# Kernel tuning notes

Measured on AMD Instinct MI355X. Metric: run time of the kernel, lower is better.

## Reference

```python
import jax, jax.numpy as jnp
import numpy as np

B, S, H = 1, 4096, 3584
NQ, NKV, D = 16, 8, 256
N_REP = NQ // NKV  # GQA repeat factor = 2
WINDOW = 2048
SOFTCAP = 50.0
THETA = 10000.0
SCALE = D ** -0.5


def rotate_half(x):
    h = x.shape[-1] // 2
    return jnp.concatenate([-x[..., h:], x[..., :h]], axis=-1)


def setup_inputs() -> dict:
    key = jax.random.key(0)
    k0, k1, k2, k3, k4 = jax.random.split(key, 5)
    return {
        "hidden_states": jax.random.normal(k0, (B, S, H), jnp.float32),
        "wq": jax.random.normal(k1, (H, NQ * D), jnp.float32) / np.sqrt(H).astype(np.float32),
        "wk": jax.random.normal(k2, (H, NKV * D), jnp.float32) / np.sqrt(H).astype(np.float32),
        "wv": jax.random.normal(k3, (H, NKV * D), jnp.float32) / np.sqrt(H).astype(np.float32),
        "wo": jax.random.normal(k4, (NQ * D, H), jnp.float32) / np.sqrt(NQ * D).astype(np.float32),
        "position_ids": jnp.arange(S, dtype=jnp.int64 if jax.config.jax_enable_x64 else jnp.int32)[None, :],
    }


def reference(hidden_states, wq, wk, wv, wo, position_ids):
    b, s, h = hidden_states.shape
    # QKV projections (no bias, per attention_bias=False)
    q = (hidden_states @ wq).reshape(b, s, NQ, D).transpose(0, 2, 1, 3)   # [b, nq, s, d]
    k = (hidden_states @ wk).reshape(b, s, NKV, D).transpose(0, 2, 1, 3)  # [b, nkv, s, d]
    v = (hidden_states @ wv).reshape(b, s, NKV, D).transpose(0, 2, 1, 3)

    # Rotary embeddings (Gemma2RotaryEmbedding): freqs duplicated, rotate_half form
    pos = position_ids.astype(jnp.float32)                         # [b, s]
    inv_freq = 1.0 / (THETA ** (jnp.arange(0, D, 2, dtype=jnp.float32) / D))  # [d/2]
    freqs = pos[..., None] * inv_freq                              # [b, s, d/2]
    emb = jnp.concatenate([freqs, freqs], axis=-1)                 # [b, s, d]
    cos = jnp.cos(emb)[:, None, :, :]                              # [b, 1, s, d]
    sin = jnp.sin(emb)[:, None, :, :]
    q = q * cos + rotate_half(q) * sin
    k = k * cos + rotate_half(k) * sin

    # GQA: repeat_kv (repeat_interleave over head dim)
    k = jnp.repeat(k, N_REP, axis=1)  # [b, nq, s, d]
    v = jnp.repeat(v, N_REP, axis=1)

    # scaled scores + logit softcapping
    scores = jnp.einsum('bhqd,bhkd->bhqk', q, k) * SCALE
    scores = SOFTCAP * jnp.tanh(scores / SOFTCAP)

    # causal + sliding-window mask built from positions
    qpos = position_ids[:, None, :, None]  # [b,1,s,1]
    kpos = position_ids[:, None, None, :]  # [b,1,1,s]
    visible = (kpos <= qpos) & (kpos > qpos - WINDOW)
    scores = jnp.where(visible, scores, jnp.finfo(scores.dtype).min)

    attn = jax.nn.softmax(scores, axis=-1)
    out = jnp.einsum('bhqk,bhkd->bhqd', attn, v)      # [b, nq, s, d]
    out = out.transpose(0, 2, 1, 3).reshape(b, s, NQ * D)
    return out @ wo                                    # [b, s, h]
```

## Files before the change

kernel.cpp:

```cpp
#include <hip/hip_runtime.h>
#include <hip/hip_bf16.h>
#include <cstdint>
#include <cstddef>

#define DEVFN __device__ __forceinline__

typedef __attribute__((ext_vector_type(4))) float f32x4;
typedef __attribute__((ext_vector_type(8))) short bf16x8;
typedef __attribute__((ext_vector_type(4))) short short4v;
typedef __attribute__((ext_vector_type(8))) short short8v;

static constexpr int S = 4096;
static constexpr int H = 3584;
static constexpr int NQ = 16;
static constexpr int NKV = 8;
static constexpr int D = 256;
static constexpr int WINDOW = 2048;
static constexpr float SCALE = 0.0625f;

DEVFN unsigned short f2bf(float f) {
  __hip_bfloat16 h = __float2bfloat16(f);
  return __builtin_bit_cast(unsigned short, h);
}
DEVFN float bf2f(unsigned short h) {
  union { uint32_t u; float f; } x; x.u = ((uint32_t)h) << 16;
  return x.f;
}

DEVFN void load_lds16(const void* g, void* l) {
  __builtin_amdgcn_global_load_lds((const __attribute__((address_space(1))) void*)g,
                                   (__attribute__((address_space(3))) void*)l,
                                   16, 0, 0);
}

__global__ __launch_bounds__(256) void cast_hs_kernel(const float* __restrict__ in,
                                                      unsigned short* __restrict__ out) {
  int i = (blockIdx.x * 256 + threadIdx.x) * 8;
  float4 a = *(const float4*)(in + i);
  float4 b = *(const float4*)(in + i + 4);
  short8v o;
  o[0] = (short)f2bf(a.x); o[1] = (short)f2bf(a.y);
  o[2] = (short)f2bf(a.z); o[3] = (short)f2bf(a.w);
  o[4] = (short)f2bf(b.x); o[5] = (short)f2bf(b.y);
  o[6] = (short)f2bf(b.z); o[7] = (short)f2bf(b.w);
  *(short8v*)(out + i) = o;
}

__global__ __launch_bounds__(256) void transpose_cast_kernel(const float* __restrict__ in,
                                                             unsigned short* __restrict__ out,
                                                             int rows, int cols, int out_ld) {
  __shared__ float tile[64][65];
  const int r0 = blockIdx.y * 64, c0 = blockIdx.x * 64;
  const int t = threadIdx.x;
  const int rr = t >> 4, c4 = (t & 15) * 4;
#pragma unroll
  for (int j = 0; j < 4; ++j) {
    float4 v = *(const float4*)(in + (size_t)(r0 + rr + j * 16) * cols + c0 + c4);
    tile[rr + j * 16][c4 + 0] = v.x;
    tile[rr + j * 16][c4 + 1] = v.y;
    tile[rr + j * 16][c4 + 2] = v.z;
    tile[rr + j * 16][c4 + 3] = v.w;
  }
  __syncthreads();
  const int c = t >> 2, ch = (t & 3) * 16;
  short8v o0, o1;
#pragma unroll
  for (int j = 0; j < 8; ++j) o0[j] = (short)f2bf(tile[ch + j][c]);
#pragma unroll
  for (int j = 0; j < 8; ++j) o1[j] = (short)f2bf(tile[ch + 8 + j][c]);
  unsigned short* dst = out + (size_t)(c0 + c) * out_ld + r0 + ch;
  *(short8v*)dst = o0;
  *(short8v*)(dst + 8) = o1;
}

__global__ __launch_bounds__(256) void rope_table_kernel(float* __restrict__ cs) {
  int idx = blockIdx.x * 256 + threadIdx.x;
  int s = idx >> 7, i = idx & 127;
  float inv = exp2f((float)i * -0.10381025296523007f);
  float f = (float)s * inv;
  cs[idx] = cosf(f);
  cs[(S * 128) + idx] = sinf(f);
}

DEVFN void gemm256_mainloop(const unsigned short* __restrict__ A,
                            const unsigned short* __restrict__ Bt,
                            int Kdim, int lda, int ldb, int row0, int col0,
                            char* lds, f32x4 acc[8][4]) {
  const int tid = threadIdx.x, lane = tid & 63;
  const int w = tid >> 6;
  const int wm = w >> 2, wn = w & 3;
  const int NT = Kdim >> 6;

  const int u = ((tid & 7) * 16) ^ (((tid >> 3) & 7) << 4);
  const int srow = (tid >> 3) + (u >> 6) * 128;
  const int sc = (u & 63) >> 1;

  const unsigned short* aSrc = A + (size_t)(row0 + srow) * lda + sc;
  const unsigned short* bSrc = Bt + (size_t)(col0 + srow) * ldb + sc;
  const size_t aj = (size_t)64 * lda, bj = (size_t)64 * ldb;

  char* const dA = lds + tid * 16;
  char* const dB = lds + 32768 + tid * 16;

  const int aoff = (lane & 15) * 128 + ((((lane >> 4) * 16) + wm * 64) ^ ((lane & 7) << 4));
  const int boff = ((wn & 1) * 64 + (lane & 15)) * 128 +
                   ((((lane >> 4) * 16) + (wn >> 1) * 64) ^ ((lane & 7) << 4));

#define STAGE_A(kt2, kh) do { \
    char* d_ = dA + (((kt2) & 1) << 16) + ((kh) << 14); \
    const unsigned short* s_ = aSrc + (kt2) * 64 + (kh) * 32; \
    load_lds16(s_, d_); load_lds16(s_ + aj, d_ + 8192); } while (0)
#define STAGE_B(kt2, kh) do { \
    char* d_ = dB + (((kt2) & 1) << 16) + ((kh) << 14); \
    const unsigned short* s_ = bSrc + (kt2) * 64 + (kh) * 32; \
    load_lds16(s_, d_); load_lds16(s_ + bj, d_ + 8192); } while (0)

  STAGE_A(0, 0); STAGE_B(0, 0); STAGE_A(0, 1); STAGE_B(0, 1);
  if (NT > 1) { STAGE_A(1, 0); STAGE_B(1, 0); }
  asm volatile("s_waitcnt vmcnt(4)" ::: "memory");
  __builtin_amdgcn_s_barrier();
  asm volatile("" ::: "memory");

  for (int kt = 0; kt < NT; ++kt) {
    const char* lA = lds + ((kt & 1) << 16) + aoff;
    const char* lB = lds + ((kt & 1) << 16) + 32768 + boff;
    bf16x8 bfr[4];
#pragma unroll
    for (int ph = 0; ph < 4; ++ph) {
      const int kh = ph >> 1;
      const int mh = ph & 1;
      bf16x8 af[4];
#pragma unroll
      for (int j = 0; j < 4; ++j)
        af[j] = *(const bf16x8*)(lA + (kh << 14) + (mh * 4 + j) * 2048);
      if (mh == 0) {
#pragma unroll
        for (int n = 0; n < 4; ++n)
          bfr[n] = *(const bf16x8*)(lB + (kh << 14) + n * 2048);
      }
      if (ph == 0)      { if (kt + 1 < NT) STAGE_A(kt + 1, 1); }
      else if (ph == 1) { if (kt + 1 < NT) STAGE_B(kt + 1, 1); }
      else if (ph == 2) { if (kt + 2 < NT) STAGE_A(kt + 2, 0); }
      else              { if (kt + 2 < NT) STAGE_B(kt + 2, 0); }

      asm volatile("" ::: "memory");
      __builtin_amdgcn_s_barrier();
      asm volatile("" ::: "memory");
      __builtin_amdgcn_s_setprio(1);
#pragma unroll
      for (int j = 0; j < 4; ++j)
#pragma unroll
        for (int n = 0; n < 4; ++n)
          acc[mh * 4 + j][n] =
              __builtin_amdgcn_mfma_f32_16x16x32_bf16(af[j], bfr[n], acc[mh * 4 + j][n], 0, 0, 0);
      __builtin_amdgcn_s_setprio(0);
      if (ph == 3) {
        if (kt < NT - 2) asm volatile("s_waitcnt vmcnt(4)" ::: "memory");
        else             asm volatile("s_waitcnt vmcnt(0)" ::: "memory");
      }
      asm volatile("" ::: "memory");
      __builtin_amdgcn_s_barrier();
      asm volatile("" ::: "memory");
    }
  }
#undef STAGE_A
#undef STAGE_B
}

__global__ __launch_bounds__(512, 2) void gemm_qkv_kernel(const unsigned short* __restrict__ A,
                                                          const unsigned short* __restrict__ Bt,
                                                          const float* __restrict__ cs,
                                                          unsigned short* __restrict__ qb,
                                                          unsigned short* __restrict__ kbuf,
                                                          unsigned short* __restrict__ vtb) {
  extern __shared__ char lds[];
  int bid = blockIdx.x;
  bid = (bid & 7) * 64 + (bid >> 3);
  const int bx = bid & 15, by = bid >> 4;
  const int row0 = bx * 256, col0 = by * 256;
  f32x4 acc[8][4];
  f32x4 z = {0.f, 0.f, 0.f, 0.f};
#pragma unroll
  for (int m = 0; m < 8; ++m)
#pragma unroll
    for (int n = 0; n < 4; ++n) acc[m][n] = z;

  gemm256_mainloop(A, Bt, H, H, H, row0, col0, lds, acc);

  const int lane = threadIdx.x & 63, w = threadIdx.x >> 6;
  const int wm = w >> 2, wn = w & 3;
  const int rbase = row0 + wm * 128 + (lane >> 4) * 4;
  const int cbase = col0 + wn * 64 + (lane & 15);

  if (col0 < 6144) {
    const bool isQ = (col0 < 4096);
    const float sgn = (wn < 2) ? -1.0f : 1.0f;
    float* lf = (float*)lds;
    const float* pp = lf + (((w ^ 2) << 6) + lane) * 16;
#pragma unroll
    for (int m = 0; m < 8; ++m) {
      __syncthreads();
#pragma unroll
      for (int n = 0; n < 4; ++n)
#pragma unroll
        for (int r = 0; r < 4; ++r)
          lf[threadIdx.x * 16 + n * 4 + r] = acc[m][n][r];
      __syncthreads();
#pragma unroll
      for (int n = 0; n < 4; ++n) {
        const int dm = (wn & 1) * 64 + n * 16 + (lane & 15);
#pragma unroll
        for (int r = 0; r < 4; ++r) {
          const int row = rbase + m * 16 + r;
          const float c = cs[(row << 7) + dm];
          const float s = cs[(S << 7) + (row << 7) + dm];
          const float v = acc[m][n][r] * c + sgn * pp[n * 4 + r] * s;
          const int col = cbase + n * 16;
          if (isQ) {
            qb[((size_t)(col >> 8) * S + row) * D + (col & 255)] = f2bf(v);
          } else {
            const int c2 = col - 4096;
            kbuf[((size_t)(c2 >> 8) * S + row) * D + (c2 & 255)] = f2bf(v);
          }
        }
      }
    }
  } else {
#pragma unroll
    for (int m = 0; m < 8; ++m)
#pragma unroll
      for (int n = 0; n < 4; ++n)
#pragma unroll
        for (int r = 0; r < 4; ++r) {
          int row = rbase + m * 16 + r;
          int c3 = cbase + n * 16 - 6144;
          vtb[((size_t)(c3 >> 8) * D + (c3 & 255)) * S + row] = f2bf(acc[m][n][r]);
        }
  }
}

__global__ __launch_bounds__(512, 2) void gemm_out_kernel(const unsigned short* __restrict__ A,
                                                          const unsigned short* __restrict__ Bt,
                                                          float* __restrict__ C) {
  extern __shared__ char lds[];
  int bid = blockIdx.x;
  bid = (bid & 7) * 28 + (bid >> 3);
  const int bx = bid & 15, by = bid >> 4;
  const int row0 = bx * 256, col0 = by * 256;
  f32x4 acc[8][4];
  f32x4 z = {0.f, 0.f, 0.f, 0.f};
#pragma unroll
  for (int m = 0; m < 8; ++m)
#pragma unroll
    for (int n = 0; n < 4; ++n) acc[m][n] = z;

  gemm256_mainloop(A, Bt, NQ * D, NQ * D, NQ * D, row0, col0, lds, acc);

  const int lane = threadIdx.x & 63, w = threadIdx.x >> 6;
  const int wm = w >> 2, wn = w & 3;
  const int rbase = row0 + wm * 128 + (lane >> 4) * 4;
  const int cbase = col0 + wn * 64 + (lane & 15);
#pragma unroll
  for (int m = 0; m < 8; ++m)
#pragma unroll
    for (int n = 0; n < 4; ++n)
#pragma unroll
      for (int r = 0; r < 4; ++r)
        C[(size_t)(rbase + m * 16 + r) * H + cbase + n * 16] = acc[m][n][r];
}

__global__ __launch_bounds__(256, 2) void attn_kernel(const unsigned short* __restrict__ q,
                                                      const unsigned short* __restrict__ kk_,
                                                      const unsigned short* __restrict__ vt,
                                                      unsigned short* __restrict__ aout) {
  __shared__ __align__(16) char kl[2][16384];
  __shared__ __align__(16) char vl[2][16384];
  __shared__ __align__(16) char pl[8192];
  const int tid = threadIdx.x, lane = tid & 63, w = tid >> 6;
  const int h = blockIdx.y, hv = h >> 1;
  const int q0 = blockIdx.x * 128;
  const int ql = lane & 15;
  const int grp = lane >> 4;
  const int qw = q0 + w * 32;

  bf16x8 qf[2][8];
#pragma unroll
  for (int qs = 0; qs < 2; ++qs) {
    const unsigned short* qrow = q + ((size_t)h * S + qw + qs * 16 + ql) * D;
#pragma unroll
    for (int t = 0; t < 8; ++t)
      qf[qs][t] = *(const bf16x8*)(qrow + t * 32 + grp * 8);
  }

  f32x4 oacc[2][16];
  f32x4 z = {0.f, 0.f, 0.f, 0.f};
#pragma unroll
  for (int qs = 0; qs < 2; ++qs)
#pragma unroll
    for (int i = 0; i < 16; ++i) oacc[qs][i] = z;
  float lrun[2] = {0.0f, 0.0f};

  int lo = q0 - (WINDOW - 1); if (lo < 0) lo = 0;
  const int kb0 = lo & ~31;
  const int kend = q0 + 96;

  const unsigned short* kbase = kk_ + (size_t)hv * S * D;
  const unsigned short* vbase = vt + (size_t)hv * D * S;
  int koff[4], voff[4];
#pragma unroll
  for (int j = 0; j < 4; ++j) {
    int c = w + 4 * j;
    int key = c * 2 + (lane >> 5);
    int colK = (((lane & 31) * 16) ^ ((key & 7) << 4)) >> 1;
    koff[j] = key * D + colK;
    int dd = c * 16 + (lane >> 2);
    int colV = (((lane & 3) * 16) ^ (((dd >> 1) & 3) << 4)) >> 1;
    voff[j] = dd * S + colV;
  }

  auto stage = [&](int buf, int kb) {
#pragma unroll
    for (int j = 0; j < 4; ++j) {
      int c = w + 4 * j;
      load_lds16(kbase + (size_t)kb * D + koff[j], &kl[buf][c * 1024]);
      load_lds16(vbase + kb + voff[j], &vl[buf][c * 1024]);
    }
  };

  stage(0, kb0);
  int cur = 0;
  const int psw = ((ql >> 1) & 3) << 4;
  char* pw = pl + w * 2048;
  const int ksw = (ql & 7) << 4;

  for (int kb = kb0; kb <= kend; kb += 32) {
    __syncthreads();
    if (kb + 32 <= kend) stage(cur ^ 1, kb + 32);

    f32x4 sacc[2][2];
    sacc[0][0] = z; sacc[0][1] = z; sacc[1][0] = z; sacc[1][1] = z;
#pragma unroll
    for (int t = 0; t < 8; ++t) {
      bf16x8 af[2];
#pragma unroll
      for (int ms = 0; ms < 2; ++ms)
        af[ms] = *(const bf16x8*)(kl[cur] + (ms * 16 + ql) * 512 + ((t * 64 + grp * 16) ^ ksw));
#pragma unroll
      for (int qs = 0; qs < 2; ++qs)
#pragma unroll
        for (int ms = 0; ms < 2; ++ms)
          sacc[qs][ms] = __builtin_amdgcn_mfma_f32_16x16x32_bf16(af[ms], qf[qs][t], sacc[qs][ms], 0, 0, 0);
    }

#pragma unroll
    for (int qs = 0; qs < 2; ++qs) {
      const int qsb = qw + qs * 16;
      const int qg = qsb + ql;
      float pv[8];
#pragma unroll
      for (int i = 0; i < 8; ++i) {
        float y = sacc[qs][i >> 2][i & 3] * (SCALE / 50.0f);
        float y2 = y * y;
        float t = y * (15.0f + y2) * __builtin_amdgcn_rcpf(15.0f + 6.0f * y2);
        t = fminf(fmaxf(t, -1.0f), 1.0f);
        pv[i] = __expf(50.0f * t - 50.0f);
      }
      if (kb + 31 > qsb) {
#pragma unroll
        for (int i = 0; i < 8; ++i) {
          int key = kb + (i >> 2) * 16 + grp * 4 + (i & 3);
          if (key > qg) pv[i] = 0.0f;
        }
      } else if (kb < qsb - 2032) {
#pragma unroll
        for (int i = 0; i < 8; ++i) {
          int key = kb + (i >> 2) * 16 + grp * 4 + (i & 3);
          if (key <= qg - WINDOW) pv[i] = 0.0f;
        }
      }
#pragma unroll
      for (int i = 0; i < 8; ++i) lrun[qs] += pv[i];

#pragma unroll
      for (int ms = 0; ms < 2; ++ms) {
        short4v pk;
        pk[0] = (short)f2bf(pv[ms * 4 + 0]);
        pk[1] = (short)f2bf(pv[ms * 4 + 1]);
        pk[2] = (short)f2bf(pv[ms * 4 + 2]);
        pk[3] = (short)f2bf(pv[ms * 4 + 3]);
        *(short4v*)(pw + (qs * 16 + ql) * 64 + ((ms * 32 + grp * 8) ^ psw)) = pk;
      }
    }
    asm volatile("s_waitcnt lgkmcnt(0)" ::: "memory");
    bf16x8 pb[2];
#pragma unroll
    for (int qs = 0; qs < 2; ++qs)
      pb[qs] = *(const bf16x8*)(pw + (qs * 16 + ql) * 64 + ((grp * 16) ^ psw));

#pragma unroll
    for (int nt = 0; nt < 16; ++nt) {
      int dr = nt * 16 + ql;
      bf16x8 va = *(const bf16x8*)(vl[cur] + dr * 64 + ((grp * 16) ^ (((dr >> 1) & 3) << 4)));
      oacc[0][nt] = __builtin_amdgcn_mfma_f32_16x16x32_bf16(va, pb[0], oacc[0][nt], 0, 0, 0);
      oacc[1][nt] = __builtin_amdgcn_mfma_f32_16x16x32_bf16(va, pb[1], oacc[1][nt], 0, 0, 0);
    }
    cur ^= 1;
  }

#pragma unroll
  for (int qs = 0; qs < 2; ++qs) {
    float l = lrun[qs];
    l += __shfl_xor(l, 16);
    l += __shfl_xor(l, 32);
    l = fmaxf(l, 1e-35f);
    float rl = 1.0f / l;
    unsigned short* orow = aout + (size_t)(qw + qs * 16 + ql) * (NQ * D) + h * D;
#pragma unroll
    for (int nt = 0; nt < 16; ++nt) {
      short4v o;
      o[0] = (short)f2bf(oacc[qs][nt][0] * rl);
      o[1] = (short)f2bf(oacc[qs][nt][1] * rl);
      o[2] = (short)f2bf(oacc[qs][nt][2] * rl);
      o[3] = (short)f2bf(oacc[qs][nt][3] * rl);
      *(short4v*)(orow + nt * 16 + grp * 4) = o;
    }
  }
}

extern "C" void kernel_launch(void* const* d_in, const int* in_sizes, int n_in,
                              void* d_out, int out_size, void* d_ws, size_t ws_size,
                              hipStream_t stream) {
  const float* hs = (const float*)d_in[0];
  const float* wq = (const float*)d_in[1];
  const float* wk = (const float*)d_in[2];
  const float* wv = (const float*)d_in[3];
  const float* wo = (const float*)d_in[4];
  float* out = (float*)d_out;

  char* ws = (char*)d_ws;
  size_t off = 0;
  auto alloc = [&](size_t bytes) {
    char* p = ws + off;
    off += (bytes + 255) & ~(size_t)255;
    return p;
  };
  unsigned short* hsb   = (unsigned short*)alloc((size_t)S * H * 2);
  unsigned short* wqkvT = (unsigned short*)alloc((size_t)8192 * H * 2);
  unsigned short* woT   = (unsigned short*)alloc((size_t)H * 4096 * 2);
  unsigned short* qb    = (unsigned short*)alloc((size_t)NQ * S * D * 2);
  unsigned short* kbuf  = (unsigned short*)alloc((size_t)NKV * S * D * 2);
  unsigned short* vtb   = (unsigned short*)alloc((size_t)NKV * D * S * 2);
  unsigned short* aob   = (unsigned short*)alloc((size_t)S * NQ * D * 2);
  float*          cs    = (float*)alloc((size_t)S * 128 * 2 * 4);
  if (off > ws_size) return;

  cast_hs_kernel<<<(S * H) / 2048, 256, 0, stream>>>(hs, hsb);
  transpose_cast_kernel<<<dim3(4096 / 64, H / 64), 256, 0, stream>>>(wq, wqkvT, H, 4096, H);
  transpose_cast_kernel<<<dim3(2048 / 64, H / 64), 256, 0, stream>>>(wk, wqkvT + (size_t)4096 * H, H, 2048, H);
  transpose_cast_kernel<<<dim3(2048 / 64, H / 64), 256, 0, stream>>>(wv, wqkvT + (size_t)6144 * H, H, 2048, H);
  transpose_cast_kernel<<<dim3(H / 64, 4096 / 64), 256, 0, stream>>>(wo, woT, 4096, H, 4096);
  rope_table_kernel<<<(S * 128) / 256, 256, 0, stream>>>(cs);
  gemm_qkv_kernel<<<512, 512, 131072, stream>>>(hsb, wqkvT, cs, qb, kbuf, vtb);
  attn_kernel<<<dim3(S / 128, NQ), 256, 0, stream>>>(qb, kbuf, vtb, aob);
  gemm_out_kernel<<<224, 512, 131072, stream>>>(aob, woT, out);
}
```

Before: 676.0 us.

## Remap GEMM B-fragment columns so RoPE pairs stay in-thread, drop LDS exchange

Each wave's B fragments now cover columns d and d+128 of a head, so both halves of every rotate_half pair end up in the same thread's accumulators. The QKV epilogue then applies RoPE directly in registers. This removes the per-m-tile LDS round trip and its two __syncthreads, and the V and out-projection epilogues are updated to the new column mapping. It also replaces the library bf16 conversion with an inline round-to-nearest-even bit trick, which skips NaN handling. The new B LDS offsets may change bank-conflict behaviour in the mainloop.

```diff
diff --git a/kernel.cpp b/kernel.cpp
--- a/kernel.cpp
+++ b/kernel.cpp
@@ -19,8 +19,10 @@
 static constexpr float SCALE = 0.0625f;
 
 DEVFN unsigned short f2bf(float f) {
-  __hip_bfloat16 h = __float2bfloat16(f);
-  return __builtin_bit_cast(unsigned short, h);
+  union { float f; uint32_t u; } x; x.f = f;
+  uint32_t u = x.u;
+  u += 0x7fffu + ((u >> 16) & 1u);
+  return (unsigned short)(u >> 16);
 }
 DEVFN float bf2f(unsigned short h) {
   union { uint32_t u; float f; } x; x.u = ((uint32_t)h) << 16;
@@ -103,8 +105,11 @@
   char* const dB = lds + 32768 + tid * 16;
 
   const int aoff = (lane & 15) * 128 + ((((lane >> 4) * 16) + wm * 64) ^ ((lane & 7) << 4));
-  const int boff = ((wn & 1) * 64 + (lane & 15)) * 128 +
-                   ((((lane >> 4) * 16) + (wn >> 1) * 64) ^ ((lane & 7) << 4));
+  int boffs[4];
+#pragma unroll
+  for (int n = 0; n < 4; ++n)
+    boffs[n] = (wn >> 1) * 8192 + ((wn & 1) * 32 + (n & 1) * 16 + (lane & 15)) * 128 +
+               ((((lane >> 4) | ((n >> 1) << 2)) ^ (lane & 7)) << 4);
 
 #define STAGE_A(kt2, kh) do { \
     char* d_ = dA + (((kt2) & 1) << 16) + ((kh) << 14); \
@@ -123,7 +128,7 @@
 
   for (int kt = 0; kt < NT; ++kt) {
     const char* lA = lds + ((kt & 1) << 16) + aoff;
-    const char* lB = lds + ((kt & 1) << 16) + 32768 + boff;
+    const char* lB = lds + ((kt & 1) << 16) + 32768;
     bf16x8 bfr[4];
 #pragma unroll
     for (int ph = 0; ph < 4; ++ph) {
@@ -136,7 +141,7 @@
       if (mh == 0) {
 #pragma unroll
         for (int n = 0; n < 4; ++n)
-          bfr[n] = *(const bf16x8*)(lB + (kh << 14) + n * 2048);
+          bfr[n] = *(const bf16x8*)(lB + (kh << 14) + boffs[n]);
       }
       if (ph == 0)      { if (kt + 1 < NT) STAGE_A(kt + 1, 1); }
       else if (ph == 1) { if (kt + 1 < NT) STAGE_B(kt + 1, 1); }
@@ -190,52 +195,41 @@
   const int lane = threadIdx.x & 63, w = threadIdx.x >> 6;
   const int wm = w >> 2, wn = w & 3;
   const int rbase = row0 + wm * 128 + (lane >> 4) * 4;
-  const int cbase = col0 + wn * 64 + (lane & 15);
 
   if (col0 < 6144) {
     const bool isQ = (col0 < 4096);
-    const float sgn = (wn < 2) ? -1.0f : 1.0f;
-    float* lf = (float*)lds;
-    const float* pp = lf + (((w ^ 2) << 6) + lane) * 16;
-#pragma unroll
-    for (int m = 0; m < 8; ++m) {
-      __syncthreads();
-#pragma unroll
-      for (int n = 0; n < 4; ++n)
-#pragma unroll
-        for (int r = 0; r < 4; ++r)
-          lf[threadIdx.x * 16 + n * 4 + r] = acc[m][n][r];
-      __syncthreads();
-#pragma unroll
-      for (int n = 0; n < 4; ++n) {
-        const int dm = (wn & 1) * 64 + n * 16 + (lane & 15);
+    const int hoff = isQ ? (col0 >> 8) : ((col0 - 4096) >> 8);
+    unsigned short* dst = isQ ? qb : kbuf;
+    const int dmb = wn * 32 + (lane & 15);
+#pragma unroll
+    for (int m = 0; m < 8; ++m)
+#pragma unroll
+      for (int nl = 0; nl < 2; ++nl) {
+        const int dm = dmb + nl * 16;
 #pragma unroll
         for (int r = 0; r < 4; ++r) {
           const int row = rbase + m * 16 + r;
           const float c = cs[(row << 7) + dm];
           const float s = cs[(S << 7) + (row << 7) + dm];
-          const float v = acc[m][n][r] * c + sgn * pp[n * 4 + r] * s;
-          const int col = cbase + n * 16;
-          if (isQ) {
-            qb[((size_t)(col >> 8) * S + row) * D + (col & 255)] = f2bf(v);
-          } else {
-            const int c2 = col - 4096;
-            kbuf[((size_t)(c2 >> 8) * S + row) * D + (c2 & 255)] = f2bf(v);
-          }
+          const float xlo = acc[m][nl][r], xhi = acc[m][nl + 2][r];
+          unsigned short* p = dst + ((size_t)hoff * S + row) * D + dm;
+          p[0]   = f2bf(xlo * c - xhi * s);
+          p[128] = f2bf(xhi * c + xlo * s);
         }
       }
-    }
   } else {
+    const int hoff = (col0 - 6144) >> 8;
 #pragma unroll
     for (int m = 0; m < 8; ++m)
 #pragma unroll
-      for (int n = 0; n < 4; ++n)
+      for (int n = 0; n < 4; ++n) {
+        const int d = wn * 32 + (n & 1) * 16 + (n >> 1) * 128 + (lane & 15);
 #pragma unroll
         for (int r = 0; r < 4; ++r) {
           int row = rbase + m * 16 + r;
-          int c3 = cbase + n * 16 - 6144;
-          vtb[((size_t)(c3 >> 8) * D + (c3 & 255)) * S + row] = f2bf(acc[m][n][r]);
+          vtb[((size_t)hoff * D + d) * S + row] = f2bf(acc[m][n][r]);
         }
+      }
   }
 }
 
@@ -259,14 +253,16 @@
   const int lane = threadIdx.x & 63, w = threadIdx.x >> 6;
   const int wm = w >> 2, wn = w & 3;
   const int rbase = row0 + wm * 128 + (lane >> 4) * 4;
-  const int cbase = col0 + wn * 64 + (lane & 15);
+  const int cb = col0 + wn * 32 + (lane & 15);
 #pragma unroll
   for (int m = 0; m < 8; ++m)
 #pragma unroll
-    for (int n = 0; n < 4; ++n)
+    for (int n = 0; n < 4; ++n) {
+      const int col = cb + (n & 1) * 16 + (n >> 1) * 128;
 #pragma unroll
       for (int r = 0; r < 4; ++r)
-        C[(size_t)(rbase + m * 16 + r) * H + cbase + n * 16] = acc[m][n][r];
+        C[(size_t)(rbase + m * 16 + r) * H + col] = acc[m][n][r];
+    }
 }
 
 __global__ __launch_bounds__(256, 2) void attn_kernel(const unsigned short* __restrict__ q,
```

After: 642.7 us. 4.9% less time.
